# Performance work log

Measured on AMD Instinct MI355X. Metric: run time of the kernel, lower is better.

## Reference

```python
import jax, jax.numpy as jnp
import numpy as np

NUM_USERS = 100000
NUM_ITEMS = 100000
N = NUM_USERS + NUM_ITEMS
D = 64
E = 1200000


def setup_inputs() -> dict:
    key = jax.random.key(0)
    k1, k2, k3, k4, k5 = jax.random.split(key, 5)
    edge_index = jax.random.randint(k1, (2, E), 0, N, dtype=jnp.int64)
    user_emb = jax.random.normal(k2, (NUM_USERS, D), dtype=jnp.float32)
    item_emb = jax.random.normal(k3, (NUM_ITEMS, D), dtype=jnp.float32)
    W1 = jax.random.normal(k4, (D, D), dtype=jnp.float32) / np.sqrt(D)
    b1 = jnp.zeros((D,), dtype=jnp.float32)
    W2 = jax.random.normal(k5, (D, D), dtype=jnp.float32) / np.sqrt(D)
    b2 = jnp.zeros((D,), dtype=jnp.float32)
    return {"edge_index": edge_index, "user_emb": user_emb, "item_emb": item_emb,
            "W1": W1, "b1": b1, "W2": W2, "b2": b2}


def _gcn_conv(x, row, col, norm, W, b, n_nodes):
    # x: [N, D]; row/col: [E+N] (with self-loops); norm: [E+N]
    x = x @ W                                  # linear transform (no bias in lin)
    msg = x[row] * norm[:, None]               # gather + scale (memory-bound)
    out = jax.ops.segment_sum(msg, col, num_segments=n_nodes)  # scatter-add
    return out + b


def reference(edge_index, user_emb, item_emb, W1, b1, W2, b2):
    x = jnp.concatenate([user_emb, item_emb], axis=0)  # [N, D]
    n_nodes = x.shape[0]
    # gcn_norm: add self-loops, symmetric deg^{-1/2} normalization
    sl = jnp.arange(n_nodes, dtype=edge_index.dtype)
    row = jnp.concatenate([edge_index[0], sl])
    col = jnp.concatenate([edge_index[1], sl])
    deg = jax.ops.segment_sum(jnp.ones_like(col, dtype=x.dtype), col,
                              num_segments=n_nodes)
    dinv = jnp.where(deg > 0, jax.lax.rsqrt(jnp.maximum(deg, 1e-12)), 0.0)
    norm = dinv[row] * dinv[col]
    x = _gcn_conv(x, row, col, norm, W1, b1, n_nodes)
    x = _gcn_conv(x, row, col, norm, W2, b2, n_nodes)
    return x
```

## Files before the change

### kernel.cpp

```cpp
#include <hip/hip_runtime.h>

#define DIM 64
#define GPW 4
#define BSHIFT 9
#define BSPAN 512
#define MAXNB 512
#define CNTB 256

typedef __attribute__((ext_vector_type(8))) __bf16 bf16x8;
typedef __attribute__((ext_vector_type(8))) unsigned short u16x8;
typedef __attribute__((ext_vector_type(4))) float f32x4;

__device__ __forceinline__ f32x4 mfma16(bf16x8 a, bf16x8 b, f32x4 c) {
    return __builtin_amdgcn_mfma_f32_16x16x32_bf16(a, b, c, 0, 0, 0);
}

__device__ __forceinline__ float bf2f(unsigned short u) {
    return __uint_as_float((unsigned)u << 16);
}


__global__ __launch_bounds__(512) void bucket_count_kernel(
    const int* __restrict__ ei, int* __restrict__ bpart, int E_, int nblk) {
    __shared__ int hist[MAXNB];
    int tid = threadIdx.x;
    int bid = blockIdx.x;
    hist[tid] = 0;
    __syncthreads();
    int chunk = (E_ + nblk - 1) / nblk;
    int e0 = bid * chunk, e1 = min(E_, e0 + chunk);
    for (int e = e0 + tid; e < e1; e += 512)
        atomicAdd(&hist[ei[E_ + e] >> BSHIFT], 1);
    __syncthreads();
    bpart[bid * MAXNB + tid] = hist[tid];
}

__global__ __launch_bounds__(512) void bucket_scan_kernel(
    const int* __restrict__ bpart, int* __restrict__ bptr,
    int* __restrict__ bcur, int* __restrict__ rowptr,
    int nblk, int N_, int E_) {
    __shared__ int sm[512];
    int tid = threadIdx.x;
    int tot = 0;
#pragma unroll 8
    for (int blk = 0; blk < nblk; ++blk)
        tot += bpart[blk * MAXNB + tid];
    sm[tid] = tot;
    __syncthreads();
    for (int off = 1; off < 512; off <<= 1) {
        int t = 0;
        if (tid >= off) t = sm[tid - off];
        __syncthreads();
        if (tid >= off) sm[tid] += t;
        __syncthreads();
    }
    int ex = sm[tid] - tot;
    bptr[tid] = ex;
    bcur[tid] = ex;
    if (tid == 0) { bptr[MAXNB] = E_; rowptr[N_] = E_; }
}

__global__ __launch_bounds__(512) void scatter_kernel(
    const int* __restrict__ ei, int* __restrict__ bcur,
    unsigned* __restrict__ packed, int E_, int nblk) {
    __shared__ int h[MAXNB];
    int tid = threadIdx.x;
    int chunk = (E_ + nblk - 1) / nblk;
    int e0 = blockIdx.x * chunk, e1 = min(E_, e0 + chunk);
    h[tid] = 0;
    __syncthreads();
    for (int e = e0 + tid; e < e1; e += 512)
        atomicAdd(&h[ei[E_ + e] >> BSHIFT], 1);
    __syncthreads();
    int c = h[tid];
    h[tid] = c ? atomicAdd(&bcur[tid], c) : 0;
    __syncthreads();
    for (int e = e0 + tid; e < e1; e += 512) {
        int s = ei[e], d = ei[E_ + e];
        int b = d >> BSHIFT;
        int pos = atomicAdd(&h[b], 1);
        packed[pos] = ((unsigned)s << BSHIFT) | (unsigned)(d & (BSPAN - 1));
    }
}

__global__ __launch_bounds__(256) void bucket_sort_kernel(
    const unsigned* __restrict__ packed, const int* __restrict__ bptr,
    int* __restrict__ rowptr, int* __restrict__ srcs,
    float* __restrict__ dinv, int N_) {
    __shared__ int cnt[BSPAN];
    __shared__ int sc[256];
    int tid = threadIdx.x;
    int b = blockIdx.x;
    int beg = bptr[b], end = bptr[b + 1];
    int node0 = b << BSHIFT;
    int nn = min(BSPAN, N_ - node0);
    cnt[tid] = 0; cnt[tid + 256] = 0;
    __syncthreads();
    for (int i = beg + tid; i < end; i += 256)
        atomicAdd(&cnt[packed[i] & (BSPAN - 1)], 1);
    __syncthreads();
    int degA = cnt[tid], degB = cnt[tid + 256];
    int a0 = cnt[2 * tid], a1 = cnt[2 * tid + 1];
    if (tid < nn) dinv[node0 + tid] = rsqrtf((float)(1 + degA));
    if (tid + 256 < nn) dinv[node0 + tid + 256] = rsqrtf((float)(1 + degB));
    int tot = a0 + a1;
    sc[tid] = tot;
    __syncthreads();
    for (int off = 1; off < 256; off <<= 1) {
        int t = 0;
        if (tid >= off) t = sc[tid - off];
        __syncthreads();
        if (tid >= off) sc[tid] += t;
        __syncthreads();
    }
    int ex = sc[tid] - tot;
    cnt[2 * tid] = ex;
    cnt[2 * tid + 1] = ex + a0;
    __syncthreads();
    if (tid < nn) rowptr[node0 + tid] = beg + cnt[tid];
    if (tid + 256 < nn) rowptr[node0 + tid + 256] = beg + cnt[tid + 256];
    __syncthreads();
    for (int i = beg + tid; i < end; i += 256) {
        unsigned p = packed[i];
        int pos = atomicAdd(&cnt[p & (BSPAN - 1)], 1);
        srcs[beg + pos] = (int)(p >> BSHIFT);
    }
}


template <bool BF16IN>
__global__ __launch_bounds__(256) void gemm_kernel(
    const void* __restrict__ xa_, const void* __restrict__ xb_, int split,
    const float* __restrict__ W, const float* __restrict__ dinv,
    __bf16* __restrict__ h, int n, int ngroups) {
    int lane = threadIdx.x & 63;
    int q = lane >> 4, t = lane & 15;
    int wv = __builtin_amdgcn_readfirstlane(threadIdx.x >> 6);
    int g0 = (blockIdx.x * 4 + wv) * GPW;
    if (g0 >= ngroups) return;

    bf16x8 Bf[4][2];
#pragma unroll
    for (int nt = 0; nt < 4; ++nt)
#pragma unroll
        for (int kt = 0; kt < 2; ++kt) {
            bf16x8 f;
#pragma unroll
            for (int j = 0; j < 8; ++j)
                f[j] = (__bf16)W[(kt * 32 + q * 8 + j) * DIM + nt * 16 + t];
            Bf[nt][kt] = f;
        }

    auto loadA = [&](int r0, f32x4* raw) {
        int row = r0 + t;
        if (row >= n) row = n - 1;
        if constexpr (BF16IN) {
            const __bf16* xr = (const __bf16*)xa_ + (size_t)row * DIM;
            raw[0] = *(const f32x4*)(xr + q * 8);
            raw[1] = *(const f32x4*)(xr + 32 + q * 8);
        } else {
            const float* xr = (row < split)
                ? ((const float*)xa_ + (size_t)row * DIM)
                : ((const float*)xb_ + (size_t)(row - split) * DIM);
            raw[0] = *(const f32x4*)(xr + q * 8);
            raw[1] = *(const f32x4*)(xr + q * 8 + 4);
            raw[2] = *(const f32x4*)(xr + 32 + q * 8);
            raw[3] = *(const f32x4*)(xr + 32 + q * 8 + 4);
        }
    };

    f32x4 cur[4];
    loadA(g0 * 16, cur);

#pragma unroll 1
    for (int gi = 0; gi < GPW; ++gi) {
        int g = g0 + gi;
        if (g >= ngroups) break;
        int r0 = g * 16;
        f32x4 nxt[4];
        bool pf = (gi + 1 < GPW) && (g + 1 < ngroups);
        if (pf) loadA(r0 + 16, nxt);

        bf16x8 A0, A1;
        if constexpr (BF16IN) {
            A0 = __builtin_bit_cast(bf16x8, cur[0]);
            A1 = __builtin_bit_cast(bf16x8, cur[1]);
        } else {
#pragma unroll
            for (int j = 0; j < 4; ++j) {
                A0[j] = (__bf16)cur[0][j]; A0[j + 4] = (__bf16)cur[1][j];
                A1[j] = (__bf16)cur[2][j]; A1[j + 4] = (__bf16)cur[3][j];
            }
        }

        f32x4 z = {0.f, 0.f, 0.f, 0.f};
        f32x4 acc[4];
#pragma unroll
        for (int nt = 0; nt < 4; ++nt)
            acc[nt] = mfma16(A1, Bf[nt][1], mfma16(A0, Bf[nt][0], z));

        f32x4 d4 = *(const f32x4*)(dinv + r0 + q * 4);
#pragma unroll
        for (int nt = 0; nt < 4; ++nt)
#pragma unroll
            for (int reg = 0; reg < 4; ++reg) {
                int row = r0 + q * 4 + reg;
                if (row < n)
                    h[(size_t)row * DIM + nt * 16 + t] =
                        (__bf16)(acc[nt][reg] * d4[reg]);
            }
#pragma unroll
        for (int i = 0; i < 4; ++i) cur[i] = nxt[i];
    }
}

template <typename OutT>
__global__ __launch_bounds__(256) void agg_kernel(
    const int* __restrict__ rowptr, const int* __restrict__ srcs,
    const __bf16* __restrict__ h, const float* __restrict__ bias,
    const float* __restrict__ dinv, OutT* __restrict__ out, int n) {
    int lane = threadIdx.x & 63;
    int t8 = lane & 7;
    int wv = threadIdx.x >> 6;
    int node = (blockIdx.x * 4 + wv) * 8 + (lane >> 3);
    bool alive = node < n;
    int nd = alive ? node : (n - 1);
    int beg = rowptr[nd], end = rowptr[nd + 1];

    u16x8 sv = *(const u16x8*)(h + (size_t)nd * DIM + t8 * 8);
    float acc[8];
#pragma unroll
    for (int j = 0; j < 8; ++j) acc[j] = bf2f(sv[j]);

    int i = beg;
    while (i < end) {
        int idx = i + t8;
        int sl = (idx < end) ? srcs[idx] : 0;
        u16x8 vv[8];
#pragma unroll
        for (int k = 0; k < 8; ++k) {
            int s = __shfl(sl, (lane & 56) | k);
            vv[k] = *(const u16x8*)(h + (size_t)s * DIM + t8 * 8);
        }
#pragma unroll
        for (int k = 0; k < 8; ++k)
            if (i + k < end) {
#pragma unroll
                for (int j = 0; j < 8; ++j) acc[j] += bf2f(vv[k][j]);
            }
        i += 8;
    }

    float dn = dinv[nd];
    f32x4 b0 = *(const f32x4*)(bias + t8 * 8);
    f32x4 b1 = *(const f32x4*)(bias + t8 * 8 + 4);
    if (alive) {
        if constexpr (sizeof(OutT) == 4) {
            f32x4 o0, o1;
#pragma unroll
            for (int j = 0; j < 4; ++j) {
                o0[j] = fmaf(dn, acc[j],     b0[j]);
                o1[j] = fmaf(dn, acc[j + 4], b1[j]);
            }
            float* op = (float*)out + (size_t)node * DIM + t8 * 8;
            *(f32x4*)op = o0;
            *(f32x4*)(op + 4) = o1;
        } else {
            bf16x8 o;
#pragma unroll
            for (int j = 0; j < 4; ++j) {
                o[j]     = (__bf16)fmaf(dn, acc[j],     b0[j]);
                o[j + 4] = (__bf16)fmaf(dn, acc[j + 4], b1[j]);
            }
            *(bf16x8*)((__bf16*)out + (size_t)node * DIM + t8 * 8) = o;
        }
    }
}

static inline size_t align16(size_t x) { return (x + 15) & ~(size_t)15; }

extern "C" void kernel_launch(void* const* d_in, const int* in_sizes, int n_in,
                              void* d_out, int out_size, void* d_ws, size_t ws_size,
                              hipStream_t stream) {
    const int* ei         = (const int*)d_in[0];
    const float* user_emb = (const float*)d_in[1];
    const float* item_emb = (const float*)d_in[2];
    const float* W1 = (const float*)d_in[3];
    const float* b1 = (const float*)d_in[4];
    const float* W2 = (const float*)d_in[5];
    const float* b2 = (const float*)d_in[6];
    float* out = (float*)d_out;

    const int E_ = in_sizes[0] / 2;
    const int NU = in_sizes[1] / DIM;
    const int NI = in_sizes[2] / DIM;
    const int N_ = NU + NI;
    const int NB = (N_ + BSPAN - 1) >> BSHIFT;

    char* p = (char*)d_ws;
    int* srcs   = (int*)p;               p += align16((size_t)E_ * 4);
    __bf16* h   = (__bf16*)p;            p += align16((size_t)N_ * DIM * 2);
    __bf16* t1  = (__bf16*)p;            p += align16((size_t)N_ * DIM * 2);
    float* dinv = (float*)p;             p += align16((size_t)N_ * 4);
    int* rowptr = (int*)p;               p += align16((size_t)(N_ + 1) * 4);
    int* bpart  = (int*)p;               p += align16((size_t)CNTB * MAXNB * 4);
    int* bptr   = (int*)p;               p += align16((size_t)(MAXNB + 1) * 4);
    int* bcur   = (int*)p;               p += align16((size_t)MAXNB * 4);
    unsigned* packed = (unsigned*)t1;

    bucket_count_kernel<<<CNTB, 512, 0, stream>>>(ei, bpart, E_, CNTB);
    bucket_scan_kernel<<<1, 512, 0, stream>>>(bpart, bptr, bcur, rowptr,
                                              CNTB, N_, E_);
    scatter_kernel<<<CNTB, 512, 0, stream>>>(ei, bcur, packed, E_, CNTB);
    bucket_sort_kernel<<<NB, 256, 0, stream>>>(packed, bptr, rowptr, srcs, dinv, N_);

    int NG = (N_ + 15) / 16;
    int gblocks = (NG + 4 * GPW - 1) / (4 * GPW);
    int ablocks = (N_ + 31) / 32;

    gemm_kernel<false><<<gblocks, 256, 0, stream>>>(user_emb, item_emb, NU,
                                                    W1, dinv, h, N_, NG);
    agg_kernel<__bf16><<<ablocks, 256, 0, stream>>>(rowptr, srcs, h, b1, dinv, t1, N_);
    gemm_kernel<true><<<gblocks, 256, 0, stream>>>(t1, t1, N_,
                                                   W2, dinv, h, N_, NG);
    agg_kernel<float><<<ablocks, 256, 0, stream>>>(rowptr, srcs, h, b2, dinv, out, N_);
}
```

Measured before the change: 254.4 us.

## Fuse first GEMM with bucket count kernel and move source scaling into aggregation

The first-layer GEMM no longer depends on dinv: it writes unscaled X@W1, and the first aggregation applies dinv[src] per edge through an extra gather and shuffle. That lets the GEMM blocks run in the same launch as the edge-bucket counting blocks, overlapping compute-bound and atomic-bound work and removing one launch from the chain. The cost is an extra dinv gather and an FMA per edge in the first aggregation. The count part now uses 256 threads per block instead of 512.

```diff
diff --git a/kernel.cpp b/kernel.cpp
--- a/kernel.cpp
+++ b/kernel.cpp
@@ -20,19 +20,99 @@
 }
 
 
-__global__ __launch_bounds__(512) void bucket_count_kernel(
-    const int* __restrict__ ei, int* __restrict__ bpart, int E_, int nblk) {
+__device__ __forceinline__ void gemm_f32_body(
+    int bid, const float* __restrict__ xa_, const float* __restrict__ xb_,
+    int split, const float* __restrict__ W, const float* __restrict__ dinv,
+    __bf16* __restrict__ h, int n, int ngroups) {
+    int lane = threadIdx.x & 63;
+    int q = lane >> 4, t = lane & 15;
+    int wv = __builtin_amdgcn_readfirstlane((threadIdx.x >> 6) & 3);
+    int g0 = (bid * 4 + wv) * GPW;
+    if (g0 >= ngroups) return;
+
+    bf16x8 Bf[4][2];
+#pragma unroll
+    for (int nt = 0; nt < 4; ++nt)
+#pragma unroll
+        for (int kt = 0; kt < 2; ++kt) {
+            bf16x8 f;
+#pragma unroll
+            for (int j = 0; j < 8; ++j)
+                f[j] = (__bf16)W[(kt * 32 + q * 8 + j) * DIM + nt * 16 + t];
+            Bf[nt][kt] = f;
+        }
+
+    auto loadA = [&](int r0, f32x4* raw) {
+        int row = r0 + t;
+        if (row >= n) row = n - 1;
+        const float* xr = (row < split)
+            ? (xa_ + (size_t)row * DIM)
+            : (xb_ + (size_t)(row - split) * DIM);
+        raw[0] = *(const f32x4*)(xr + q * 8);
+        raw[1] = *(const f32x4*)(xr + q * 8 + 4);
+        raw[2] = *(const f32x4*)(xr + 32 + q * 8);
+        raw[3] = *(const f32x4*)(xr + 32 + q * 8 + 4);
+    };
+
+    f32x4 cur[4];
+    loadA(g0 * 16, cur);
+
+#pragma unroll 1
+    for (int gi = 0; gi < GPW; ++gi) {
+        int g = g0 + gi;
+        if (g >= ngroups) break;
+        int r0 = g * 16;
+        f32x4 nxt[4];
+        bool pf = (gi + 1 < GPW) && (g + 1 < ngroups);
+        if (pf) loadA(r0 + 16, nxt);
+
+        bf16x8 A0, A1;
+#pragma unroll
+        for (int j = 0; j < 4; ++j) {
+            A0[j] = (__bf16)cur[0][j]; A0[j + 4] = (__bf16)cur[1][j];
+            A1[j] = (__bf16)cur[2][j]; A1[j + 4] = (__bf16)cur[3][j];
+        }
+
+        f32x4 z = {0.f, 0.f, 0.f, 0.f};
+        f32x4 acc[4];
+#pragma unroll
+        for (int nt = 0; nt < 4; ++nt)
+            acc[nt] = mfma16(A1, Bf[nt][1], mfma16(A0, Bf[nt][0], z));
+
+#pragma unroll
+        for (int nt = 0; nt < 4; ++nt)
+#pragma unroll
+            for (int reg = 0; reg < 4; ++reg) {
+                int row = r0 + q * 4 + reg;
+                if (row < n)
+                    h[(size_t)row * DIM + nt * 16 + t] = (__bf16)acc[nt][reg];
+            }
+#pragma unroll
+        for (int i = 0; i < 4; ++i) cur[i] = nxt[i];
+    }
+}
+
+
+__global__ __launch_bounds__(256) void count_gemm_kernel(
+    const int* __restrict__ ei, int* __restrict__ bpart, int E_,
+    const float* __restrict__ ua, const float* __restrict__ ub, int split,
+    const float* __restrict__ W1, __bf16* __restrict__ h, int n, int ngroups) {
+    if (blockIdx.x >= CNTB) {
+        gemm_f32_body(blockIdx.x - CNTB, ua, ub, split, W1, nullptr, h, n, ngroups);
+        return;
+    }
     __shared__ int hist[MAXNB];
     int tid = threadIdx.x;
     int bid = blockIdx.x;
-    hist[tid] = 0;
-    __syncthreads();
-    int chunk = (E_ + nblk - 1) / nblk;
+    hist[tid] = 0; hist[tid + 256] = 0;
+    __syncthreads();
+    int chunk = (E_ + CNTB - 1) / CNTB;
     int e0 = bid * chunk, e1 = min(E_, e0 + chunk);
-    for (int e = e0 + tid; e < e1; e += 512)
+    for (int e = e0 + tid; e < e1; e += 256)
         atomicAdd(&hist[ei[E_ + e] >> BSHIFT], 1);
     __syncthreads();
     bpart[bid * MAXNB + tid] = hist[tid];
+    bpart[bid * MAXNB + tid + 256] = hist[tid + 256];
 }
 
 __global__ __launch_bounds__(512) void bucket_scan_kernel(
@@ -128,11 +208,9 @@
 }
 
 
-template <bool BF16IN>
-__global__ __launch_bounds__(256) void gemm_kernel(
-    const void* __restrict__ xa_, const void* __restrict__ xb_, int split,
-    const float* __restrict__ W, const float* __restrict__ dinv,
-    __bf16* __restrict__ h, int n, int ngroups) {
+__global__ __launch_bounds__(256) void gemm_bf16_kernel(
+    const __bf16* __restrict__ x, const float* __restrict__ W,
+    const float* __restrict__ dinv, __bf16* __restrict__ h, int n, int ngroups) {
     int lane = threadIdx.x & 63;
     int q = lane >> 4, t = lane & 15;
     int wv = __builtin_amdgcn_readfirstlane(threadIdx.x >> 6);
@@ -154,22 +232,12 @@
     auto loadA = [&](int r0, f32x4* raw) {
         int row = r0 + t;
         if (row >= n) row = n - 1;
-        if constexpr (BF16IN) {
-            const __bf16* xr = (const __bf16*)xa_ + (size_t)row * DIM;
-            raw[0] = *(const f32x4*)(xr + q * 8);
-            raw[1] = *(const f32x4*)(xr + 32 + q * 8);
-        } else {
-            const float* xr = (row < split)
-                ? ((const float*)xa_ + (size_t)row * DIM)
-                : ((const float*)xb_ + (size_t)(row - split) * DIM);
-            raw[0] = *(const f32x4*)(xr + q * 8);
-            raw[1] = *(const f32x4*)(xr + q * 8 + 4);
-            raw[2] = *(const f32x4*)(xr + 32 + q * 8);
-            raw[3] = *(const f32x4*)(xr + 32 + q * 8 + 4);
-        }
+        const __bf16* xr = x + (size_t)row * DIM;
+        raw[0] = *(const f32x4*)(xr + q * 8);
+        raw[1] = *(const f32x4*)(xr + 32 + q * 8);
     };
 
-    f32x4 cur[4];
+    f32x4 cur[2];
     loadA(g0 * 16, cur);
 
 #pragma unroll 1
@@ -177,21 +245,12 @@
         int g = g0 + gi;
         if (g >= ngroups) break;
         int r0 = g * 16;
-        f32x4 nxt[4];
+        f32x4 nxt[2];
         bool pf = (gi + 1 < GPW) && (g + 1 < ngroups);
         if (pf) loadA(r0 + 16, nxt);
 
-        bf16x8 A0, A1;
-        if constexpr (BF16IN) {
-            A0 = __builtin_bit_cast(bf16x8, cur[0]);
-            A1 = __builtin_bit_cast(bf16x8, cur[1]);
-        } else {
-#pragma unroll
-            for (int j = 0; j < 4; ++j) {
-                A0[j] = (__bf16)cur[0][j]; A0[j + 4] = (__bf16)cur[1][j];
-                A1[j] = (__bf16)cur[2][j]; A1[j + 4] = (__bf16)cur[3][j];
-            }
-        }
+        bf16x8 A0 = __builtin_bit_cast(bf16x8, cur[0]);
+        bf16x8 A1 = __builtin_bit_cast(bf16x8, cur[1]);
 
         f32x4 z = {0.f, 0.f, 0.f, 0.f};
         f32x4 acc[4];
@@ -209,12 +268,11 @@
                     h[(size_t)row * DIM + nt * 16 + t] =
                         (__bf16)(acc[nt][reg] * d4[reg]);
             }
-#pragma unroll
-        for (int i = 0; i < 4; ++i) cur[i] = nxt[i];
-    }
-}
-
-template <typename OutT>
+        cur[0] = nxt[0]; cur[1] = nxt[1];
+    }
+}
+
+template <typename OutT, bool SRC_SCALE>
 __global__ __launch_bounds__(256) void agg_kernel(
     const int* __restrict__ rowptr, const int* __restrict__ srcs,
     const __bf16* __restrict__ h, const float* __restrict__ bias,
@@ -226,16 +284,20 @@
     bool alive = node < n;
     int nd = alive ? node : (n - 1);
     int beg = rowptr[nd], end = rowptr[nd + 1];
+    float dn = dinv[nd];
 
     u16x8 sv = *(const u16x8*)(h + (size_t)nd * DIM + t8 * 8);
+    float selfscale = SRC_SCALE ? dn : 1.f;
     float acc[8];
 #pragma unroll
-    for (int j = 0; j < 8; ++j) acc[j] = bf2f(sv[j]);
+    for (int j = 0; j < 8; ++j) acc[j] = bf2f(sv[j]) * selfscale;
 
     int i = beg;
     while (i < end) {
         int idx = i + t8;
         int sl = (idx < end) ? srcs[idx] : 0;
+        float dsl = 0.f;
+        if (SRC_SCALE && idx < end) dsl = dinv[sl];
         u16x8 vv[8];
 #pragma unroll
         for (int k = 0; k < 8; ++k) {
@@ -245,13 +307,15 @@
 #pragma unroll
         for (int k = 0; k < 8; ++k)
             if (i + k < end) {
-#pragma unroll
-                for (int j = 0; j < 8; ++j) acc[j] += bf2f(vv[k][j]);
+                float w = SRC_SCALE ? __shfl(dsl, (lane & 56) | k) : 1.f;
+#pragma unroll
+                for (int j = 0; j < 8; ++j)
+                    acc[j] = SRC_SCALE ? fmaf(bf2f(vv[k][j]), w, acc[j])
+                                       : (acc[j] + bf2f(vv[k][j]));
             }
         i += 8;
     }
 
-    float dn = dinv[nd];
     f32x4 b0 = *(const f32x4*)(bias + t8 * 8);
     f32x4 b1 = *(const f32x4*)(bias + t8 * 8 + 4);
     if (alive) {
@@ -308,20 +372,20 @@
     int* bcur   = (int*)p;               p += align16((size_t)MAXNB * 4);
     unsigned* packed = (unsigned*)t1;
 
-    bucket_count_kernel<<<CNTB, 512, 0, stream>>>(ei, bpart, E_, CNTB);
+    int NG = (N_ + 15) / 16;
+    int gblocks = (NG + 4 * GPW - 1) / (4 * GPW);
+    int ablocks = (N_ + 31) / 32;
+
+    count_gemm_kernel<<<CNTB + gblocks, 256, 0, stream>>>(
+        ei, bpart, E_, user_emb, item_emb, NU, W1, h, N_, NG);
     bucket_scan_kernel<<<1, 512, 0, stream>>>(bpart, bptr, bcur, rowptr,
                                               CNTB, N_, E_);
     scatter_kernel<<<CNTB, 512, 0, stream>>>(ei, bcur, packed, E_, CNTB);
     bucket_sort_kernel<<<NB, 256, 0, stream>>>(packed, bptr, rowptr, srcs, dinv, N_);
 
-    int NG = (N_ + 15) / 16;
-    int gblocks = (NG + 4 * GPW - 1) / (4 * GPW);
-    int ablocks = (N_ + 31) / 32;
-
-    gemm_kernel<false><<<gblocks, 256, 0, stream>>>(user_emb, item_emb, NU,
-                                                    W1, dinv, h, N_, NG);
-    agg_kernel<__bf16><<<ablocks, 256, 0, stream>>>(rowptr, srcs, h, b1, dinv, t1, N_);
-    gemm_kernel<true><<<gblocks, 256, 0, stream>>>(t1, t1, N_,
-                                                   W2, dinv, h, N_, NG);
-    agg_kernel<float><<<ablocks, 256, 0, stream>>>(rowptr, srcs, h, b2, dinv, out, N_);
-}
+    agg_kernel<__bf16, true><<<ablocks, 256, 0, stream>>>(rowptr, srcs, h, b1,
+                                                          dinv, t1, N_);
+    gemm_bf16_kernel<<<gblocks, 256, 0, stream>>>(t1, W2, dinv, h, N_, NG);
+    agg_kernel<float, false><<<ablocks, 256, 0, stream>>>(rowptr, srcs, h, b2,
+                                                          dinv, out, N_);
+}
```

New measurement: 247.1 us. 2.9% less time.
